# Kernel tuning notes

Hardware: AMD Instinct MI355X
Metric: run time of the kernel (lower is better)

The kernel has to match this reference:

```python
import jax, jax.numpy as jnp
import numpy as np

GRID_SIZE = 300


def setup_inputs() -> dict:
    key = jax.random.key(0)
    k1, k2 = jax.random.split(key)
    N, input_dim, out_dim = 2048, 256, 256
    x = jax.random.normal(k1, (N, input_dim), dtype=jnp.float32)
    scale = 1.0 / (np.sqrt(input_dim) * np.sqrt(GRID_SIZE))
    coeffs = jax.random.normal(k2, (2, out_dim, input_dim, GRID_SIZE), dtype=jnp.float32) * scale
    bias = jnp.zeros((1, out_dim), dtype=jnp.float32)
    return {"x": x, "coeffs": coeffs, "bias": bias}


def reference(x, coeffs, bias):
    # x: [N, I]; coeffs: [2, J, I, K]; bias: [1, J]
    grid_size = coeffs.shape[-1]
    k = jnp.arange(1, grid_size + 1, dtype=x.dtype)            # [K]
    ang = x[:, :, None] * k                                    # [N, I, K]
    c = jnp.cos(ang)
    s = jnp.sin(ang)
    # einsum('dbik,djik->bj') with d=2 split into cos/sin parts
    y = jnp.einsum('bik,jik->bj', c, coeffs[0]) + jnp.einsum('bik,jik->bj', s, coeffs[1])
    y = y + bias
    return y
```

## Files before the change

kernel.cpp:

```cpp
#include <hip/hip_runtime.h>
#include <stdint.h>

#define NB 2048
#define NI 256
#define NJ 256
#define GK 300
#define KPAD 320
#define KK_PER_I (2*KPAD)
#define NKC (NI*KK_PER_I/32)
#define CH_PER_I 20
#define SPLITK 32
#define II_PER_S (NI / SPLITK)
#define BM 128

typedef __bf16 bf16x8 __attribute__((ext_vector_type(8)));
typedef __bf16 bf16x2 __attribute__((ext_vector_type(2)));
typedef float  f32x4  __attribute__((ext_vector_type(4)));

__device__ __forceinline__ void sincos2pi(float ang, float& c, float& s) {
  float r = ang * 0.15915494309189535f;
  r = r - floorf(r);
  c = __builtin_amdgcn_cosf(r);
  s = __builtin_amdgcn_sinf(r);
}

__device__ __forceinline__ unsigned int pkbf(float c, float s) {
  bf16x2 p; p.x = (__bf16)c; p.y = (__bf16)s;
  return __builtin_bit_cast(unsigned int, p);
}

__device__ __forceinline__ void rot(float& c, float& s, float cr, float sr) {
  float nc = c * cr - s * sr;
  s = s * cr + c * sr;
  c = nc;
}

__global__ __launch_bounds__(256) void convert_b(const float* __restrict__ coeffs,
                                                 unsigned int* __restrict__ bw) {
  const int bid = blockIdx.x;
  const int i  = bid >> 4;
  const int jt = bid & 15;
  const int t  = (int)threadIdx.x;
  const int n  = t & 15;
  const int gl = t >> 4;
  const int j  = jt * 16 + n;

  const float4* r0 = (const float4*)(coeffs + (size_t)(j * NI + i) * GK);
  const float4* r1 = (const float4*)(coeffs + (size_t)((NJ + j) * NI + i) * GK);

  #pragma unroll
  for (int p = 0; p < 5; p++) {
    const int g = p * 16 + gl;
    uint4 w = {0u, 0u, 0u, 0u};
    if (g < GK / 4) {
      float4 a = r0[g];
      float4 b = r1[g];
      w.x = pkbf(a.x, b.x);
      w.y = pkbf(a.y, b.y);
      w.z = pkbf(a.z, b.z);
      w.w = pkbf(a.w, b.w);
    }
    const int kc = i * 20 + (g >> 2);
    const unsigned int idx = ((unsigned int)(kc * 16 + jt) << 8) + ((g & 3) << 6) + (n << 2);
    *(uint4*)(bw + idx) = w;
  }
}

__global__ __launch_bounds__(256) void init_out(const float* __restrict__ bias,
                                                float* __restrict__ out) {
  const int tid = blockIdx.x * 256 + threadIdx.x;
  float4 b = ((const float4*)bias)[tid & 63];
  ((float4*)out)[tid] = b;
}

__global__ __launch_bounds__(256, 2) void fkan_gemm(const float* __restrict__ x,
                                                    const uint4* __restrict__ bw4,
                                                    float* __restrict__ out) {
  const int bid = blockIdx.x;
  const int mt = bid & 15;
  const int s  = bid >> 4;
  const int m0 = mt * BM;

  const int t    = (int)threadIdx.x;
  const int lane = t & 63;
  const int wave = t >> 6;
  const int wr = wave >> 1;
  const int wc = wave & 1;
  const int q  = lane >> 4;
  const int ln = lane & 15;

  f32x4 acc[4][8];
  #pragma unroll
  for (int mm = 0; mm < 4; mm++)
    #pragma unroll
    for (int nn = 0; nn < 8; nn++)
      acc[mm][nn] = (f32x4){0.f, 0.f, 0.f, 0.f};

  const uint4* bptr = bw4 + (size_t)(wc * 8) * 64 + lane;

  int kc = s * (NKC / SPLITK);
  uint4 bcur[8], bnxt[8];
  #pragma unroll
  for (int nn = 0; nn < 8; nn++) bcur[nn] = bptr[(size_t)kc * 1024 + nn * 64];

  float stc[4], sts[4], c1a[4], s1a[4], cDa[4], sDa[4];

  #pragma unroll 1
  for (int ii = 0; ii < II_PER_S; ii++) {
    const int i = s * II_PER_S + ii;
    #pragma unroll
    for (int mm = 0; mm < 4; mm++) {
      const float xv = x[(m0 + wr * 64 + mm * 16 + ln) * NI + i];
      sincos2pi(xv, c1a[mm], s1a[mm]);
      sincos2pi(13.f * xv, cDa[mm], sDa[mm]);
      sincos2pi(xv * (float)(q * 4 + 1), stc[mm], sts[mm]);
    }

    #pragma unroll 2
    for (int c = 0; c < CH_PER_I; c++) {
      const int kcn = (kc + 1 < NKC) ? kc + 1 : kc;
      #pragma unroll
      for (int nn = 0; nn < 8; nn++)
        bnxt[nn] = bptr[(size_t)kcn * 1024 + nn * 64];

      bf16x8 af[4];
      #pragma unroll
      for (int mm = 0; mm < 4; mm++) {
        float cc = stc[mm], ss = sts[mm];
        uint4 u;
        u.x = pkbf(cc, ss);
        rot(cc, ss, c1a[mm], s1a[mm]); u.y = pkbf(cc, ss);
        rot(cc, ss, c1a[mm], s1a[mm]); u.z = pkbf(cc, ss);
        rot(cc, ss, c1a[mm], s1a[mm]); u.w = pkbf(cc, ss);
        rot(cc, ss, cDa[mm], sDa[mm]); stc[mm] = cc; sts[mm] = ss;
        af[mm] = __builtin_bit_cast(bf16x8, u);
      }

      #pragma unroll
      for (int nn = 0; nn < 8; nn++) {
        const bf16x8 bfr = __builtin_bit_cast(bf16x8, bcur[nn]);
        #pragma unroll
        for (int mm = 0; mm < 4; mm++)
          acc[mm][nn] = __builtin_amdgcn_mfma_f32_16x16x32_bf16(
              af[mm], bfr, acc[mm][nn], 0, 0, 0);
      }

      #pragma unroll
      for (int nn = 0; nn < 8; nn++) bcur[nn] = bnxt[nn];
      kc++;
    }
  }

  const int r0 = m0 + wr * 64 + q * 4;
  const int c0 = wc * 128 + ln;
  #pragma unroll
  for (int mm = 0; mm < 4; mm++)
    #pragma unroll
    for (int nn = 0; nn < 8; nn++)
      #pragma unroll
      for (int r = 0; r < 4; r++)
        atomicAdd(&out[(r0 + mm * 16 + r) * NJ + c0 + nn * 16], acc[mm][nn][r]);
}

extern "C" void kernel_launch(void* const* d_in, const int* in_sizes, int n_in,
                              void* d_out, int out_size, void* d_ws, size_t ws_size,
                              hipStream_t stream) {
  const float* x      = (const float*)d_in[0];
  const float* coeffs = (const float*)d_in[1];
  const float* bias   = (const float*)d_in[2];
  float* out = (float*)d_out;
  unsigned int* bw = (unsigned int*)d_ws;

  convert_b<<<dim3(NI * 16), dim3(256), 0, stream>>>(coeffs, bw);
  init_out<<<dim3(NB * NJ / 4 / 256), dim3(256), 0, stream>>>(bias, out);
  fkan_gemm<<<dim3(16 * SPLITK), dim3(256), 0, stream>>>(x, (const uint4*)bw, out);
}
```

Measured before the change: 435.4 us.

## Switch GEMM to 32x32x16 bf16 MFMA with matching B layout

Replaces the 16x16x32 MFMA tiling with 32x32x16 MFMA instructions. Each wave now covers 64x128 using 2x4 accumulators of 16 floats, and the B workspace layout produced by convert_b is rewritten to match the new fragment shape. The larger MFMA halves the number of sin/cos starting states per lane and increases reuse per instruction. The cost is a more complex A-fragment recurrence with 5x rotation steps and a different atomic output mapping.

```diff
diff --git a/kernel.cpp b/kernel.cpp
--- a/kernel.cpp
+++ b/kernel.cpp
@@ -7,15 +7,15 @@
 #define GK 300
 #define KPAD 320
 #define KK_PER_I (2*KPAD)
-#define NKC (NI*KK_PER_I/32)
-#define CH_PER_I 20
+#define NKC2 (NI*KK_PER_I/16)
+#define CH32_PER_I 20
 #define SPLITK 32
 #define II_PER_S (NI / SPLITK)
 #define BM 128
 
 typedef __bf16 bf16x8 __attribute__((ext_vector_type(8)));
 typedef __bf16 bf16x2 __attribute__((ext_vector_type(2)));
-typedef float  f32x4  __attribute__((ext_vector_type(4)));
+typedef float  f32x16 __attribute__((ext_vector_type(16)));
 
 __device__ __forceinline__ void sincos2pi(float ang, float& c, float& s) {
   float r = ang * 0.15915494309189535f;
@@ -36,21 +36,21 @@
 }
 
 __global__ __launch_bounds__(256) void convert_b(const float* __restrict__ coeffs,
-                                                 unsigned int* __restrict__ bw) {
+                                                 uint4* __restrict__ bw4) {
   const int bid = blockIdx.x;
-  const int i  = bid >> 4;
-  const int jt = bid & 15;
+  const int i  = bid >> 3;
+  const int jt = bid & 7;
   const int t  = (int)threadIdx.x;
-  const int n  = t & 15;
-  const int gl = t >> 4;
-  const int j  = jt * 16 + n;
+  const int n2 = t & 31;
+  const int gl = t >> 5;
+  const int j  = jt * 32 + n2;
 
   const float4* r0 = (const float4*)(coeffs + (size_t)(j * NI + i) * GK);
   const float4* r1 = (const float4*)(coeffs + (size_t)((NJ + j) * NI + i) * GK);
 
   #pragma unroll
-  for (int p = 0; p < 5; p++) {
-    const int g = p * 16 + gl;
+  for (int p = 0; p < 10; p++) {
+    const int g = p * 8 + gl;
     uint4 w = {0u, 0u, 0u, 0u};
     if (g < GK / 4) {
       float4 a = r0[g];
@@ -60,9 +60,8 @@
       w.z = pkbf(a.z, b.z);
       w.w = pkbf(a.w, b.w);
     }
-    const int kc = i * 20 + (g >> 2);
-    const unsigned int idx = ((unsigned int)(kc * 16 + jt) << 8) + ((g & 3) << 6) + (n << 2);
-    *(uint4*)(bw + idx) = w;
+    const int kc2 = i * 40 + (g >> 1);
+    bw4[(size_t)(kc2 * 8 + jt) * 64 + n2 + 32 * (g & 1)] = w;
   }
 }
 
@@ -86,80 +85,93 @@
   const int wave = t >> 6;
   const int wr = wave >> 1;
   const int wc = wave & 1;
-  const int q  = lane >> 4;
-  const int ln = lane & 15;
+  const int q2 = lane >> 5;
+  const int ln = lane & 31;
 
-  f32x4 acc[4][8];
+  f32x16 acc[2][4];
   #pragma unroll
-  for (int mm = 0; mm < 4; mm++)
+  for (int mm = 0; mm < 2; mm++)
     #pragma unroll
-    for (int nn = 0; nn < 8; nn++)
-      acc[mm][nn] = (f32x4){0.f, 0.f, 0.f, 0.f};
+    for (int nn = 0; nn < 4; nn++)
+      #pragma unroll
+      for (int r = 0; r < 16; r++)
+        acc[mm][nn][r] = 0.f;
 
-  const uint4* bptr = bw4 + (size_t)(wc * 8) * 64 + lane;
+  const uint4* bp = bw4 + (size_t)(wc * 4) * 64 + lane;
 
-  int kc = s * (NKC / SPLITK);
+  int kc2 = s * (NKC2 / SPLITK);
   uint4 bcur[8], bnxt[8];
   #pragma unroll
-  for (int nn = 0; nn < 8; nn++) bcur[nn] = bptr[(size_t)kc * 1024 + nn * 64];
+  for (int q = 0; q < 8; q++)
+    bcur[q] = bp[(size_t)(kc2 + (q >> 2)) * 512 + (q & 3) * 64];
 
-  float stc[4], sts[4], c1a[4], s1a[4], cDa[4], sDa[4];
+  float stc[2], sts[2], c1a[2], s1a[2], c5a[2], s5a[2];
 
   #pragma unroll 1
   for (int ii = 0; ii < II_PER_S; ii++) {
     const int i = s * II_PER_S + ii;
     #pragma unroll
-    for (int mm = 0; mm < 4; mm++) {
-      const float xv = x[(m0 + wr * 64 + mm * 16 + ln) * NI + i];
+    for (int mm = 0; mm < 2; mm++) {
+      const float xv = x[(m0 + wr * 64 + mm * 32 + ln) * NI + i];
       sincos2pi(xv, c1a[mm], s1a[mm]);
-      sincos2pi(13.f * xv, cDa[mm], sDa[mm]);
-      sincos2pi(xv * (float)(q * 4 + 1), stc[mm], sts[mm]);
+      sincos2pi(5.f * xv, c5a[mm], s5a[mm]);
+      sincos2pi(xv * (float)(q2 * 4 + 1), stc[mm], sts[mm]);
     }
 
     #pragma unroll 2
-    for (int c = 0; c < CH_PER_I; c++) {
-      const int kcn = (kc + 1 < NKC) ? kc + 1 : kc;
+    for (int c = 0; c < CH32_PER_I; c++) {
+      const int kc2n = (kc2 + 2 <= NKC2 - 2) ? kc2 + 2 : kc2;
       #pragma unroll
-      for (int nn = 0; nn < 8; nn++)
-        bnxt[nn] = bptr[(size_t)kcn * 1024 + nn * 64];
+      for (int q = 0; q < 8; q++)
+        bnxt[q] = bp[(size_t)(kc2n + (q >> 2)) * 512 + (q & 3) * 64];
 
-      bf16x8 af[4];
+      bf16x8 af[2][2];
       #pragma unroll
-      for (int mm = 0; mm < 4; mm++) {
+      for (int mm = 0; mm < 2; mm++) {
         float cc = stc[mm], ss = sts[mm];
-        uint4 u;
-        u.x = pkbf(cc, ss);
-        rot(cc, ss, c1a[mm], s1a[mm]); u.y = pkbf(cc, ss);
-        rot(cc, ss, c1a[mm], s1a[mm]); u.z = pkbf(cc, ss);
-        rot(cc, ss, c1a[mm], s1a[mm]); u.w = pkbf(cc, ss);
-        rot(cc, ss, cDa[mm], sDa[mm]); stc[mm] = cc; sts[mm] = ss;
-        af[mm] = __builtin_bit_cast(bf16x8, u);
+        uint4 u0, u1;
+        u0.x = pkbf(cc, ss);
+        rot(cc, ss, c1a[mm], s1a[mm]); u0.y = pkbf(cc, ss);
+        rot(cc, ss, c1a[mm], s1a[mm]); u0.z = pkbf(cc, ss);
+        rot(cc, ss, c1a[mm], s1a[mm]); u0.w = pkbf(cc, ss);
+        rot(cc, ss, c5a[mm], s5a[mm]);
+        u1.x = pkbf(cc, ss);
+        rot(cc, ss, c1a[mm], s1a[mm]); u1.y = pkbf(cc, ss);
+        rot(cc, ss, c1a[mm], s1a[mm]); u1.z = pkbf(cc, ss);
+        rot(cc, ss, c1a[mm], s1a[mm]); u1.w = pkbf(cc, ss);
+        rot(cc, ss, c5a[mm], s5a[mm]);
+        stc[mm] = cc; sts[mm] = ss;
+        af[mm][0] = __builtin_bit_cast(bf16x8, u0);
+        af[mm][1] = __builtin_bit_cast(bf16x8, u1);
       }
 
       #pragma unroll
-      for (int nn = 0; nn < 8; nn++) {
-        const bf16x8 bfr = __builtin_bit_cast(bf16x8, bcur[nn]);
+      for (int ks = 0; ks < 2; ks++)
         #pragma unroll
-        for (int mm = 0; mm < 4; mm++)
-          acc[mm][nn] = __builtin_amdgcn_mfma_f32_16x16x32_bf16(
-              af[mm], bfr, acc[mm][nn], 0, 0, 0);
-      }
+        for (int nn = 0; nn < 4; nn++) {
+          const bf16x8 bfr = __builtin_bit_cast(bf16x8, bcur[ks * 4 + nn]);
+          #pragma unroll
+          for (int mm = 0; mm < 2; mm++)
+            acc[mm][nn] = __builtin_amdgcn_mfma_f32_32x32x16_bf16(
+                af[mm][ks], bfr, acc[mm][nn], 0, 0, 0);
+        }
 
       #pragma unroll
-      for (int nn = 0; nn < 8; nn++) bcur[nn] = bnxt[nn];
-      kc++;
+      for (int q = 0; q < 8; q++) bcur[q] = bnxt[q];
+      kc2 += 2;
     }
   }
 
-  const int r0 = m0 + wr * 64 + q * 4;
-  const int c0 = wc * 128 + ln;
+  const int cb = wc * 128 + ln;
   #pragma unroll
-  for (int mm = 0; mm < 4; mm++)
+  for (int mm = 0; mm < 2; mm++)
     #pragma unroll
-    for (int nn = 0; nn < 8; nn++)
+    for (int nn = 0; nn < 4; nn++)
       #pragma unroll
-      for (int r = 0; r < 4; r++)
-        atomicAdd(&out[(r0 + mm * 16 + r) * NJ + c0 + nn * 16], acc[mm][nn][r]);
+      for (int r = 0; r < 16; r++) {
+        const int row = m0 + wr * 64 + mm * 32 + (r & 3) + 8 * (r >> 2) + 4 * q2;
+        atomicAdd(&out[row * NJ + cb + nn * 32], acc[mm][nn][r]);
+      }
 }
 
 extern "C" void kernel_launch(void* const* d_in, const int* in_sizes, int n_in,
@@ -169,9 +181,9 @@
   const float* coeffs = (const float*)d_in[1];
   const float* bias   = (const float*)d_in[2];
   float* out = (float*)d_out;
-  unsigned int* bw = (unsigned int*)d_ws;
+  uint4* bw4 = (uint4*)d_ws;
 
-  convert_b<<<dim3(NI * 16), dim3(256), 0, stream>>>(coeffs, bw);
+  convert_b<<<dim3(NI * 8), dim3(256), 0, stream>>>(coeffs, bw4);
   init_out<<<dim3(NB * NJ / 4 / 256), dim3(256), 0, stream>>>(bias, out);
-  fkan_gemm<<<dim3(16 * SPLITK), dim3(256), 0, stream>>>(x, (const uint4*)bw, out);
+  fkan_gemm<<<dim3(16 * SPLITK), dim3(256), 0, stream>>>(x, (const uint4*)bw4, out);
 }
```

Result: slower. 448.0 us (+2.9%).
